# Kernel tuning notes

Measured on AMD Instinct MI355X. Metric: run time of the kernel, lower is better.

Reference implementation:

```python
import jax, jax.numpy as jnp
import numpy as np

NEG_BIG = -9e15
ALPHA = 0.2  # LeakyReLU negative slope


def setup_inputs() -> dict:
    key = jax.random.key(0)
    k1, k2, k3, k4 = jax.random.split(key, 4)
    N, F_in, F_out = 8192, 256, 64
    inp = jax.random.normal(k1, (N, F_in), dtype=jnp.float32)
    adj = jax.random.randint(k2, (N, N), 0, 2, dtype=jnp.int32)
    W = jax.random.normal(k3, (F_in, F_out), dtype=jnp.float32) * 0.05
    a = jax.random.normal(k4, (2 * F_out, 1), dtype=jnp.float32) * 0.05
    return {"input": inp, "adj": adj, "W": W, "a": a}


def reference(input, adj, W, a):
    # h = X W : [N, F_out]
    h = input @ W
    F_out = W.shape[1]
    # a_input[i,j] = concat(h_i, h_j); a_input @ a = h@a1 broadcast over j + h@a2 broadcast over i.
    a1 = a[:F_out, 0]   # [F_out]
    a2 = a[F_out:, 0]   # [F_out]
    s1 = h @ a1         # [N]
    s2 = h @ a2         # [N]
    e = jax.nn.leaky_relu(s1[:, None] + s2[None, :], negative_slope=ALPHA)  # [N, N]
    att = jnp.where(adj > 0, e, jnp.float32(NEG_BIG))
    att = jax.nn.softmax(att, axis=1)
    # dropout is identity in eval mode (training=False)
    h_prime = att @ h   # [N, F_out]
    return jax.nn.elu(h_prime)
```

## Files before the change

kernel.cpp:

```cpp
#include <hip/hip_runtime.h>
#include <hip/hip_bf16.h>

typedef __bf16 bf16_t;
typedef __attribute__((ext_vector_type(8))) __bf16 bf16x8;
typedef __attribute__((ext_vector_type(4))) __bf16 bf16x4;
typedef __attribute__((ext_vector_type(4))) float floatx4;
typedef __attribute__((ext_vector_type(4))) int intx4;
typedef __attribute__((ext_vector_type(4))) unsigned int uintx4;

#define NN 8192
#define FIN 256
#define FOUT 64
#define GAT_ALPHA 0.2f
#define JSPLIT 8
#define JSEG (NN / JSPLIT)
#define NSTEP (JSEG / 32)

__global__ __launch_bounds__(256) void gat_h_kernel(
    const float* __restrict__ input,
    const float* __restrict__ W,
    const float* __restrict__ a,
    bf16_t* __restrict__ hT,
    float* __restrict__ e1g, float* __restrict__ f1g,
    unsigned* __restrict__ ef2g)
{
    alignas(16) __shared__ bf16_t in_lds[32][264];
    alignas(16) __shared__ bf16_t wt_lds[64][264];
    __shared__ float h_lds[32][65];

    const int t  = threadIdx.x;
    const int i0 = blockIdx.x * 32;

    #pragma unroll
    for (int v = 0; v < 8; v++) {
        int u  = v * 256 + t;
        int i  = u >> 6;
        int k4 = (u & 63) * 4;
        floatx4 x = *(const floatx4*)(input + (size_t)(i0 + i) * FIN + k4);
        bf16x4 b;
        #pragma unroll
        for (int e = 0; e < 4; e++) b[e] = (bf16_t)x[e];
        *(bf16x4*)(&in_lds[i][k4]) = b;
    }
    #pragma unroll
    for (int v = 0; v < 16; v++) {
        int u  = v * 256 + t;
        int k  = u >> 4;
        int f4 = (u & 15) * 4;
        floatx4 wv = *(const floatx4*)(W + k * FOUT + f4);
        #pragma unroll
        for (int e = 0; e < 4; e++) wt_lds[f4 + e][k] = (bf16_t)wv[e];
    }
    __syncthreads();

    const int wave = t >> 6;
    const int lane = t & 63;
    const int i16  = (wave & 1) * 16;
    const int f32  = (wave >> 1) * 32;
    const int lm   = lane & 15;
    const int lq   = lane >> 4;

    floatx4 acc0 = {0.f, 0.f, 0.f, 0.f};
    floatx4 acc1 = {0.f, 0.f, 0.f, 0.f};
    #pragma unroll
    for (int ks = 0; ks < 8; ks++) {
        int ko = ks * 32 + lq * 8;
        bf16x8 af = *(const bf16x8*)(&in_lds[i16 + lm][ko]);
        bf16x8 b0 = *(const bf16x8*)(&wt_lds[f32 + lm][ko]);
        bf16x8 b1 = *(const bf16x8*)(&wt_lds[f32 + 16 + lm][ko]);
        acc0 = __builtin_amdgcn_mfma_f32_16x16x32_bf16(af, b0, acc0, 0, 0, 0);
        acc1 = __builtin_amdgcn_mfma_f32_16x16x32_bf16(af, b1, acc1, 0, 0, 0);
    }

    #pragma unroll
    for (int c = 0; c < 2; c++) {
        floatx4 acc = c ? acc1 : acc0;
        int f  = f32 + c * 16 + lm;
        int ib = i0 + i16 + lq * 4;
        bf16x4 hp;
        #pragma unroll
        for (int r = 0; r < 4; r++) hp[r] = (bf16_t)acc[r];
        *(bf16x4*)(hT + (size_t)f * NN + ib) = hp;
    }
    #pragma unroll
    for (int c = 0; c < 2; c++) {
        floatx4 acc = c ? acc1 : acc0;
        #pragma unroll
        for (int r = 0; r < 4; r++)
            h_lds[i16 + lq * 4 + r][f32 + c * 16 + lm] = acc[r];
    }
    __syncthreads();

    if (t < 64) {
        int r   = t & 31;
        int sel = t >> 5;
        const float* av = a + sel * FOUT;
        float s = 0.f;
        #pragma unroll 8
        for (int f = 0; f < FOUT; f++) s += h_lds[r][f] * av[f];
        int gi = i0 + r;
        float E = expf(s);
        float F = expf(GAT_ALPHA * s);
        if (sel == 0) {
            e1g[gi] = E; f1g[gi] = F;
        } else {
            unsigned eb = __builtin_bit_cast(unsigned short, (bf16_t)E);
            unsigned fb = __builtin_bit_cast(unsigned short, (bf16_t)F);
            ef2g[gi] = (fb << 16) | eb;
        }
    }
}

#define LOADS(B, OFF)                                                          \
    {                                                                          \
        adjb[B][0] = *(const intx4*)(adjrow + (OFF));                          \
        adjb[B][1] = *(const intx4*)(adjrow + (OFF) + 4);                      \
        efb[B][0]  = *(const uintx4*)(efp + (OFF));                            \
        efb[B][1]  = *(const uintx4*)(efp + (OFF) + 4);                        \
        _Pragma("unroll")                                                      \
        for (int c = 0; c < 4; c++)                                            \
            htb[B][c] = *(const bf16x8*)(htp + (size_t)c * 16 * NN + (OFF));   \
    }

#define CONSUME(B)                                                             \
    {                                                                          \
        bf16x8 wf;                                                             \
        _Pragma("unroll")                                                      \
        for (int e = 0; e < 8; e++) {                                          \
            int av      = (e < 4) ? adjb[B][0][e] : adjb[B][1][e - 4];         \
            unsigned v  = (e < 4) ? efb[B][0][e] : efb[B][1][e - 4];           \
            float e2 = __builtin_bit_cast(float, v << 16);                     \
            float f2 = __builtin_bit_cast(float, v & 0xffff0000u);             \
            float p  = fmaxf(E1 * e2, F1 * f2);                                \
            float wv = (av > 0) ? p : 0.f;                                     \
            bf16_t wb = (bf16_t)wv;                                            \
            wf[e] = wb;                                                        \
            rowsum += (float)wb;                                               \
        }                                                                      \
        _Pragma("unroll")                                                      \
        for (int c = 0; c < 4; c++)                                            \
            acc[c] = __builtin_amdgcn_mfma_f32_16x16x32_bf16(                  \
                wf, htb[B][c], acc[c], 0, 0, 0);                               \
    }

__global__ __launch_bounds__(256, 4) void gat_att_kernel(
    const int* __restrict__ adj,
    const bf16_t* __restrict__ hT,
    const float* __restrict__ e1g, const float* __restrict__ f1g,
    const unsigned* __restrict__ ef2g,
    float* __restrict__ pacc,
    float* __restrict__ prs)
{
    const int t    = threadIdx.x;
    const int wave = t >> 6;
    const int lane = t & 63;
    const int m    = lane & 15;
    const int q    = lane >> 4;
    const int i0   = blockIdx.x * 64 + wave * 16;
    const int js   = blockIdx.y;
    const int row  = i0 + m;

    const float E1 = e1g[row];
    const float F1 = f1g[row];

    const int*      adjrow = adj + (size_t)row * NN + js * JSEG + q * 8;
    const unsigned* efp    = ef2g + js * JSEG + q * 8;
    const bf16_t*   htp    = hT + (size_t)m * NN + js * JSEG + q * 8;

    floatx4 acc[4];
    #pragma unroll
    for (int c = 0; c < 4; c++) acc[c] = (floatx4){0.f, 0.f, 0.f, 0.f};
    float rowsum = 0.f;

    intx4  adjb[2][2];
    uintx4 efb[2][2];
    bf16x8 htb[2][4];

    LOADS(0, 0);
    for (int s = 0; s < NSTEP; s += 2) {
        LOADS(1, (s + 1) * 32);
        CONSUME(0);
        if (s + 2 < NSTEP) LOADS(0, (s + 2) * 32);
        CONSUME(1);
    }

    rowsum += __shfl_xor(rowsum, 16, 64);
    rowsum += __shfl_xor(rowsum, 32, 64);
    if (lane < 16) prs[(size_t)js * NN + i0 + lane] = rowsum;

    float* pa = pacc + (size_t)js * NN * FOUT;
    #pragma unroll
    for (int c = 0; c < 4; c++) {
        #pragma unroll
        for (int r = 0; r < 4; r++)
            pa[(size_t)(i0 + q * 4 + r) * FOUT + c * 16 + m] = acc[c][r];
    }
}

__global__ __launch_bounds__(256) void gat_combine_kernel(
    const float* __restrict__ pacc,
    const float* __restrict__ prs,
    float* __restrict__ out)
{
    int idx = blockIdx.x * 256 + threadIdx.x;
    int i   = idx >> 4;
    floatx4 s = {0.f, 0.f, 0.f, 0.f};
    float rs  = 0.f;
    #pragma unroll
    for (int js = 0; js < JSPLIT; js++) {
        s  += *(const floatx4*)(pacc + (size_t)js * NN * FOUT + (size_t)idx * 4);
        rs += prs[(size_t)js * NN + i];
    }
    float rinv = (rs > 0.f) ? 1.0f / rs : 0.f;
    floatx4 r;
    #pragma unroll
    for (int e = 0; e < 4; e++) {
        float x = s[e] * rinv;
        r[e] = (x > 0.f) ? x : (expf(x) - 1.0f);
    }
    *(floatx4*)(out + (size_t)idx * 4) = r;
}

extern "C" void kernel_launch(void* const* d_in, const int* in_sizes, int n_in,
                              void* d_out, int out_size, void* d_ws, size_t ws_size,
                              hipStream_t stream) {
    const float* input = (const float*)d_in[0];
    const int*   adj   = (const int*)d_in[1];
    const float* W     = (const float*)d_in[2];
    const float* a     = (const float*)d_in[3];
    float*       out   = (float*)d_out;

    char* ws = (char*)d_ws;
    bf16_t*   hT   = (bf16_t*)ws;
    float*    e1g  = (float*)(ws + (1 << 20));
    float*    f1g  = e1g + NN;
    unsigned* ef2g = (unsigned*)(f1g + NN);
    float*    pacc = (float*)(ef2g + NN);
    float*    prs  = pacc + (size_t)JSPLIT * NN * FOUT;

    gat_h_kernel<<<NN / 32, 256, 0, stream>>>(input, W, a, hT, e1g, f1g, ef2g);

    dim3 gridB(NN / 64, JSPLIT);
    gat_att_kernel<<<gridB, 256, 0, stream>>>(adj, hT, e1g, f1g, ef2g,
                                              pacc, prs);

    gat_combine_kernel<<<NN * FOUT / 4 / 256, 256, 0, stream>>>(pacc, prs, out);
}
```

Before: 417.8 us.

## Stage adjacency tiles into LDS via direct global-to-LDS loads per wave

The attention kernel no longer reads adjacency rows into registers with strided per-lane vector loads. Each wave now issues global_load_lds transfers that copy 256-column chunks of 16 adjacency rows into its own LDS region, then reads the mask values back from LDS. The bias/exp terms and hT fragments are still prefetched into registers in a rotating pair, and a manual waitcnt gates each chunk. Blocks shrink to 128 threads with a matching grid change. The staging is single-buffered per wave, so the next chunk's transfer is exposed at the start of each iteration, and the larger LDS footprint lowers occupancy.

```diff
diff --git a/kernel.cpp b/kernel.cpp
--- a/kernel.cpp
+++ b/kernel.cpp
@@ -6,7 +6,8 @@
 typedef __attribute__((ext_vector_type(4))) __bf16 bf16x4;
 typedef __attribute__((ext_vector_type(4))) float floatx4;
 typedef __attribute__((ext_vector_type(4))) int intx4;
-typedef __attribute__((ext_vector_type(4))) unsigned int uintx4;
+typedef __attribute__((ext_vector_type(4))) unsigned uintx4;
+typedef __attribute__((ext_vector_type(2))) unsigned uint2v;
 
 #define NN 8192
 #define FIN 256
@@ -14,7 +15,10 @@
 #define GAT_ALPHA 0.2f
 #define JSPLIT 8
 #define JSEG (NN / JSPLIT)
-#define NSTEP (JSEG / 32)
+#define CHUNKJ 256
+#define NCHUNK (JSEG / CHUNKJ)
+#define SUBSTRIDE 264
+#define WAVE_LDS (64 * SUBSTRIDE)
 
 __global__ __launch_bounds__(256) void gat_h_kernel(
     const float* __restrict__ input,
@@ -111,39 +115,34 @@
     }
 }
 
-#define LOADS(B, OFF)                                                          \
+#define ISSUE_DMA(C)                                                           \
     {                                                                          \
-        adjb[B][0] = *(const intx4*)(adjrow + (OFF));                          \
-        adjb[B][1] = *(const intx4*)(adjrow + (OFF) + 4);                      \
-        efb[B][0]  = *(const uintx4*)(efp + (OFF));                            \
-        efb[B][1]  = *(const uintx4*)(efp + (OFF) + 4);                        \
         _Pragma("unroll")                                                      \
-        for (int c = 0; c < 4; c++)                                            \
-            htb[B][c] = *(const bf16x8*)(htp + (size_t)c * 16 * NN + (OFF));   \
-    }
-
-#define CONSUME(B)                                                             \
+        for (int mm = 0; mm < 16; mm++) {                                      \
+            const int* gsrc = adj + (size_t)(i0 + mm) * NN + jbase             \
+                              + (C) * CHUNKJ + lane;                           \
+            _Pragma("unroll")                                                  \
+            for (int g = 0; g < 4; g++) {                                      \
+                __builtin_amdgcn_global_load_lds(                              \
+                    (const __attribute__((address_space(1))) unsigned*)        \
+                        (gsrc + g * 64),                                       \
+                    (__attribute__((address_space(3))) unsigned*)              \
+                        (lbase + (g * 16 + mm) * SUBSTRIDE),                   \
+                    4, 0, 0);                                                  \
+            }                                                                  \
+        }                                                                      \
+    }
+
+#define PREFETCH(P, JLOC)                                                      \
     {                                                                          \
-        bf16x8 wf;                                                             \
+        efb[P][0] = *(const uintx4*)(efp + (JLOC));                            \
+        efb[P][1] = *(const uintx4*)(efp + (JLOC) + 4);                        \
         _Pragma("unroll")                                                      \
-        for (int e = 0; e < 8; e++) {                                          \
-            int av      = (e < 4) ? adjb[B][0][e] : adjb[B][1][e - 4];         \
-            unsigned v  = (e < 4) ? efb[B][0][e] : efb[B][1][e - 4];           \
-            float e2 = __builtin_bit_cast(float, v << 16);                     \
-            float f2 = __builtin_bit_cast(float, v & 0xffff0000u);             \
-            float p  = fmaxf(E1 * e2, F1 * f2);                                \
-            float wv = (av > 0) ? p : 0.f;                                     \
-            bf16_t wb = (bf16_t)wv;                                            \
-            wf[e] = wb;                                                        \
-            rowsum += (float)wb;                                               \
-        }                                                                      \
-        _Pragma("unroll")                                                      \
-        for (int c = 0; c < 4; c++)                                            \
-            acc[c] = __builtin_amdgcn_mfma_f32_16x16x32_bf16(                  \
-                wf, htb[B][c], acc[c], 0, 0, 0);                               \
-    }
-
-__global__ __launch_bounds__(256, 4) void gat_att_kernel(
+        for (int cc = 0; cc < 4; cc++)                                         \
+            htb[P][cc] = *(const bf16x8*)(htp + (size_t)cc * 16 * NN + (JLOC));\
+    }
+
+__global__ __launch_bounds__(128, 2) void gat_att_kernel(
     const int* __restrict__ adj,
     const bf16_t* __restrict__ hT,
     const float* __restrict__ e1g, const float* __restrict__ f1g,
@@ -151,37 +150,79 @@
     float* __restrict__ pacc,
     float* __restrict__ prs)
 {
-    const int t    = threadIdx.x;
-    const int wave = t >> 6;
-    const int lane = t & 63;
-    const int m    = lane & 15;
-    const int q    = lane >> 4;
-    const int i0   = blockIdx.x * 64 + wave * 16;
-    const int js   = blockIdx.y;
-    const int row  = i0 + m;
+    __shared__ char alds[2][WAVE_LDS];
+
+    const int t     = threadIdx.x;
+    const int wave  = t >> 6;
+    const int lane  = t & 63;
+    const int m     = lane & 15;
+    const int q     = lane >> 4;
+    const int i0    = blockIdx.x * 32 + wave * 16;
+    const int js    = blockIdx.y;
+    const int jbase = js * JSEG;
+    const int row   = i0 + m;
+
+    char* lbase = alds[wave];
 
     const float E1 = e1g[row];
     const float F1 = f1g[row];
 
-    const int*      adjrow = adj + (size_t)row * NN + js * JSEG + q * 8;
-    const unsigned* efp    = ef2g + js * JSEG + q * 8;
-    const bf16_t*   htp    = hT + (size_t)m * NN + js * JSEG + q * 8;
+    ISSUE_DMA(0);
+
+    const unsigned* efp = ef2g + jbase + q * 8;
+    const bf16_t*   htp = hT + (size_t)m * NN + jbase + q * 8;
 
     floatx4 acc[4];
     #pragma unroll
     for (int c = 0; c < 4; c++) acc[c] = (floatx4){0.f, 0.f, 0.f, 0.f};
     float rowsum = 0.f;
 
-    intx4  adjb[2][2];
+    bf16x8 htb[2][4];
     uintx4 efb[2][2];
-    bf16x8 htb[2][4];
-
-    LOADS(0, 0);
-    for (int s = 0; s < NSTEP; s += 2) {
-        LOADS(1, (s + 1) * 32);
-        CONSUME(0);
-        if (s + 2 < NSTEP) LOADS(0, (s + 2) * 32);
-        CONSUME(1);
+
+    for (int c = 0; c < NCHUNK; c++) {
+        const int jc = c * CHUNKJ;
+        PREFETCH(0, jc);
+        PREFETCH(1, jc + 32);
+        __builtin_amdgcn_s_waitcnt(0x0F7C);
+
+        #pragma unroll
+        for (int s = 0; s < 8; s++) {
+            const char* lsrc = lbase + (((s >> 1) * 16 + m) * SUBSTRIDE)
+                               + ((s & 1) * 128) + (q * 32);
+            uint2v a0 = *(const uint2v*)(lsrc);
+            uint2v a1 = *(const uint2v*)(lsrc + 8);
+            uint2v a2 = *(const uint2v*)(lsrc + 16);
+            uint2v a3 = *(const uint2v*)(lsrc + 24);
+            int adji[8];
+            adji[0] = (int)a0.x; adji[1] = (int)a0.y;
+            adji[2] = (int)a1.x; adji[3] = (int)a1.y;
+            adji[4] = (int)a2.x; adji[5] = (int)a2.y;
+            adji[6] = (int)a3.x; adji[7] = (int)a3.y;
+
+            const int p = s & 1;
+            bf16x8 wf;
+            #pragma unroll
+            for (int e = 0; e < 8; e++) {
+                unsigned v = (e < 4) ? efb[p][0][e] : efb[p][1][e - 4];
+                float e2 = __builtin_bit_cast(float, v << 16);
+                float f2 = __builtin_bit_cast(float, v & 0xffff0000u);
+                float pv = fmaxf(E1 * e2, F1 * f2);
+                float wv = (adji[e] > 0) ? pv : 0.f;
+                bf16_t wb = (bf16_t)wv;
+                wf[e] = wb;
+                rowsum += (float)wb;
+            }
+            bf16x8 hb0 = htb[p][0], hb1 = htb[p][1],
+                   hb2 = htb[p][2], hb3 = htb[p][3];
+            if (s < 6) PREFETCH(p, jc + (s + 2) * 32);
+            acc[0] = __builtin_amdgcn_mfma_f32_16x16x32_bf16(wf, hb0, acc[0], 0, 0, 0);
+            acc[1] = __builtin_amdgcn_mfma_f32_16x16x32_bf16(wf, hb1, acc[1], 0, 0, 0);
+            acc[2] = __builtin_amdgcn_mfma_f32_16x16x32_bf16(wf, hb2, acc[2], 0, 0, 0);
+            acc[3] = __builtin_amdgcn_mfma_f32_16x16x32_bf16(wf, hb3, acc[3], 0, 0, 0);
+        }
+        __builtin_amdgcn_sched_barrier(0);
+        if (c + 1 < NCHUNK) ISSUE_DMA(c + 1);
     }
 
     rowsum += __shfl_xor(rowsum, 16, 64);
@@ -240,8 +281,8 @@
 
     gat_h_kernel<<<NN / 32, 256, 0, stream>>>(input, W, a, hT, e1g, f1g, ef2g);
 
-    dim3 gridB(NN / 64, JSPLIT);
-    gat_att_kernel<<<gridB, 256, 0, stream>>>(adj, hT, e1g, f1g, ef2g,
+    dim3 gridB(NN / 32, JSPLIT);
+    gat_att_kernel<<<gridB, 128, 0, stream>>>(adj, hT, e1g, f1g, ef2g,
                                               pacc, prs);
 
     gat_combine_kernel<<<NN * FOUT / 4 / 256, 256, 0, stream>>>(pacc, prs, out);
```

Measured after the change: 446.5 us. 6.9% more time.

## Stage adjacency rows through LDS with coalesced row-wise loads and register prefetch

Applied to the files above, without the earlier changes.

The attention kernel now loads adjacency tiles with fully coalesced row-contiguous 16-byte loads (each wave reads 16 rows × 256 columns per phase) into padded per-wave LDS buffers. The next phase is prefetched into registers while the current one is consumed, and e2/hT loads are software-pipelined across k-steps. The j-split is halved and blocks shrink to 2 waves. The aim is to fix the scattered per-lane row access to the 256 MB adjacency stream and make it bandwidth-efficient, at the cost of heavy register use (16 intx4 held in flight) and lower occupancy.

```diff
diff --git a/kernel.cpp b/kernel.cpp
--- a/kernel.cpp
+++ b/kernel.cpp
@@ -6,15 +6,17 @@
 typedef __attribute__((ext_vector_type(4))) __bf16 bf16x4;
 typedef __attribute__((ext_vector_type(4))) float floatx4;
 typedef __attribute__((ext_vector_type(4))) int intx4;
-typedef __attribute__((ext_vector_type(4))) unsigned int uintx4;
+typedef __attribute__((ext_vector_type(4))) unsigned uintx4;
 
 #define NN 8192
 #define FIN 256
 #define FOUT 64
 #define GAT_ALPHA 0.2f
-#define JSPLIT 8
+#define JSPLIT 4
 #define JSEG (NN / JSPLIT)
-#define NSTEP (JSEG / 32)
+#define PHASEJ 256
+#define NPHASE (JSEG / PHASEJ)
+#define ADJ_STRIDE 260
 
 __global__ __launch_bounds__(256) void gat_h_kernel(
     const float* __restrict__ input,
@@ -111,39 +113,7 @@
     }
 }
 
-#define LOADS(B, OFF)                                                          \
-    {                                                                          \
-        adjb[B][0] = *(const intx4*)(adjrow + (OFF));                          \
-        adjb[B][1] = *(const intx4*)(adjrow + (OFF) + 4);                      \
-        efb[B][0]  = *(const uintx4*)(efp + (OFF));                            \
-        efb[B][1]  = *(const uintx4*)(efp + (OFF) + 4);                        \
-        _Pragma("unroll")                                                      \
-        for (int c = 0; c < 4; c++)                                            \
-            htb[B][c] = *(const bf16x8*)(htp + (size_t)c * 16 * NN + (OFF));   \
-    }
-
-#define CONSUME(B)                                                             \
-    {                                                                          \
-        bf16x8 wf;                                                             \
-        _Pragma("unroll")                                                      \
-        for (int e = 0; e < 8; e++) {                                          \
-            int av      = (e < 4) ? adjb[B][0][e] : adjb[B][1][e - 4];         \
-            unsigned v  = (e < 4) ? efb[B][0][e] : efb[B][1][e - 4];           \
-            float e2 = __builtin_bit_cast(float, v << 16);                     \
-            float f2 = __builtin_bit_cast(float, v & 0xffff0000u);             \
-            float p  = fmaxf(E1 * e2, F1 * f2);                                \
-            float wv = (av > 0) ? p : 0.f;                                     \
-            bf16_t wb = (bf16_t)wv;                                            \
-            wf[e] = wb;                                                        \
-            rowsum += (float)wb;                                               \
-        }                                                                      \
-        _Pragma("unroll")                                                      \
-        for (int c = 0; c < 4; c++)                                            \
-            acc[c] = __builtin_amdgcn_mfma_f32_16x16x32_bf16(                  \
-                wf, htb[B][c], acc[c], 0, 0, 0);                               \
-    }
-
-__global__ __launch_bounds__(256, 4) void gat_att_kernel(
+__global__ __launch_bounds__(128, 2) void gat_att_kernel(
     const int* __restrict__ adj,
     const bf16_t* __restrict__ hT,
     const float* __restrict__ e1g, const float* __restrict__ f1g,
@@ -151,37 +121,92 @@
     float* __restrict__ pacc,
     float* __restrict__ prs)
 {
+    __shared__ int alds[2][16 * ADJ_STRIDE];
+
     const int t    = threadIdx.x;
     const int wave = t >> 6;
     const int lane = t & 63;
     const int m    = lane & 15;
     const int q    = lane >> 4;
-    const int i0   = blockIdx.x * 64 + wave * 16;
+    const int i0   = blockIdx.x * 32 + wave * 16;
     const int js   = blockIdx.y;
+    const int jb   = js * JSEG;
     const int row  = i0 + m;
+
+    int* lds = alds[wave];
 
     const float E1 = e1g[row];
     const float F1 = f1g[row];
 
-    const int*      adjrow = adj + (size_t)row * NN + js * JSEG + q * 8;
-    const unsigned* efp    = ef2g + js * JSEG + q * 8;
-    const bf16_t*   htp    = hT + (size_t)m * NN + js * JSEG + q * 8;
-
     floatx4 acc[4];
     #pragma unroll
     for (int c = 0; c < 4; c++) acc[c] = (floatx4){0.f, 0.f, 0.f, 0.f};
     float rowsum = 0.f;
 
-    intx4  adjb[2][2];
-    uintx4 efb[2][2];
-    bf16x8 htb[2][4];
-
-    LOADS(0, 0);
-    for (int s = 0; s < NSTEP; s += 2) {
-        LOADS(1, (s + 1) * 32);
-        CONSUME(0);
-        if (s + 2 < NSTEP) LOADS(0, (s + 2) * 32);
-        CONSUME(1);
+    intx4 g[16];
+    #pragma unroll
+    for (int r = 0; r < 16; r++)
+        g[r] = *(const intx4*)(adj + (size_t)(i0 + r) * NN + jb + 4 * lane);
+
+    for (int p = 0; p < NPHASE; p++) {
+        __builtin_amdgcn_s_waitcnt(0xC07F);
+
+        #pragma unroll
+        for (int r = 0; r < 16; r++)
+            *(intx4*)(lds + r * ADJ_STRIDE + 4 * lane) = g[r];
+
+        if (p + 1 < NPHASE) {
+            #pragma unroll
+            for (int r = 0; r < 16; r++)
+                g[r] = *(const intx4*)(adj + (size_t)(i0 + r) * NN + jb
+                                       + (p + 1) * PHASEJ + 4 * lane);
+        }
+
+        const unsigned* efp = ef2g + jb + p * PHASEJ + q * 8;
+        const bf16_t*   htp = hT + (size_t)m * NN + jb + p * PHASEJ + q * 8;
+        const int*      ap  = lds + m * ADJ_STRIDE + q * 8;
+
+        uintx4 e0 = *(const uintx4*)(efp);
+        uintx4 e1 = *(const uintx4*)(efp + 4);
+        bf16x8 hb[4];
+        #pragma unroll
+        for (int c = 0; c < 4; c++)
+            hb[c] = *(const bf16x8*)(htp + (size_t)c * 16 * NN);
+
+        #pragma unroll
+        for (int ks = 0; ks < 8; ks++) {
+            intx4 a0 = *(const intx4*)(ap + ks * 32);
+            intx4 a1 = *(const intx4*)(ap + ks * 32 + 4);
+
+            uintx4 ce0 = e0, ce1 = e1;
+            bf16x8 chb0 = hb[0], chb1 = hb[1], chb2 = hb[2], chb3 = hb[3];
+            if (ks < 7) {
+                e0 = *(const uintx4*)(efp + (ks + 1) * 32);
+                e1 = *(const uintx4*)(efp + (ks + 1) * 32 + 4);
+                #pragma unroll
+                for (int c = 0; c < 4; c++)
+                    hb[c] = *(const bf16x8*)(htp + (size_t)c * 16 * NN
+                                             + (ks + 1) * 32);
+            }
+
+            bf16x8 wf;
+            #pragma unroll
+            for (int e = 0; e < 8; e++) {
+                int av     = (e < 4) ? a0[e] : a1[e - 4];
+                unsigned v = (e < 4) ? ce0[e] : ce1[e - 4];
+                float e2 = __builtin_bit_cast(float, v << 16);
+                float f2 = __builtin_bit_cast(float, v & 0xffff0000u);
+                float pv = fmaxf(E1 * e2, F1 * f2);
+                float wv = (av > 0) ? pv : 0.f;
+                bf16_t wb = (bf16_t)wv;
+                wf[e] = wb;
+                rowsum += (float)wb;
+            }
+            acc[0] = __builtin_amdgcn_mfma_f32_16x16x32_bf16(wf, chb0, acc[0], 0, 0, 0);
+            acc[1] = __builtin_amdgcn_mfma_f32_16x16x32_bf16(wf, chb1, acc[1], 0, 0, 0);
+            acc[2] = __builtin_amdgcn_mfma_f32_16x16x32_bf16(wf, chb2, acc[2], 0, 0, 0);
+            acc[3] = __builtin_amdgcn_mfma_f32_16x16x32_bf16(wf, chb3, acc[3], 0, 0, 0);
+        }
     }
 
     rowsum += __shfl_xor(rowsum, 16, 64);
@@ -240,8 +265,8 @@
 
     gat_h_kernel<<<NN / 32, 256, 0, stream>>>(input, W, a, hT, e1g, f1g, ef2g);
 
-    dim3 gridB(NN / 64, JSPLIT);
-    gat_att_kernel<<<gridB, 256, 0, stream>>>(adj, hT, e1g, f1g, ef2g,
+    dim3 gridB(NN / 32, JSPLIT);
+    gat_att_kernel<<<gridB, 128, 0, stream>>>(adj, hT, e1g, f1g, ef2g,
                                               pacc, prs);
 
     gat_combine_kernel<<<NN * FOUT / 4 / 256, 256, 0, stream>>>(pacc, prs, out);
```

Result: faster. 400.4 us (-4.2%).
